# Kernel optimization log

Hardware: AMD Instinct MI355X
Metric: run time of the kernel (lower is better)

Reference implementation:

```python
import jax, jax.numpy as jnp
import numpy as np

B = 2
ROW, COL = 63, 84          # resolution
ROW_, COL_ = 32, 42        # resolution_
N = ROW * COL              # 5292 kv tokens
N_ = ROW_ * COL_           # 1344 q tokens
IN_DIM, OUT_DIM = 256, 512
KEY_DIM, NUM_HEADS, ATTN_RATIO, STRIDE = 16, 8, 2, 2
D = ATTN_RATIO * KEY_DIM   # 32 (value dim per head)
DH = D * NUM_HEADS         # 256
NH_KD = KEY_DIM * NUM_HEADS  # 128
H_KV = DH + NH_KD          # 384
SCALE = KEY_DIM ** -0.5
EPS = 1e-5


def _build_bias_idxs():
    # replicates the itertools.product double loop, vectorized; ids ordered by
    # first occurrence in row-major scan (same as dict insertion order).
    r_ = np.arange(ROW_); c_ = np.arange(COL_)
    r = np.arange(ROW); c = np.arange(COL)
    off_r = np.abs(r_[:, None] * STRIDE - r[None, :])      # (32, 63)
    off_c = np.abs(c_[:, None] * STRIDE - c[None, :])      # (42, 84)
    keys = (off_r[:, None, :, None] * 1000 + off_c[None, :, None, :]).reshape(-1)
    _, first_idx, inv = np.unique(keys, return_index=True, return_inverse=True)
    order = np.argsort(first_idx)
    rank = np.empty_like(order); rank[order] = np.arange(len(order))
    idxs = rank[inv].reshape(N_, N).astype(np.int32)
    return idxs, len(order)


def setup_inputs() -> dict:
    key = jax.random.key(0)
    ks = jax.random.split(key, 12)
    idxs_np, n_off = _build_bias_idxs()
    inp = {
        "x": jax.random.normal(ks[0], (B, N, IN_DIM), jnp.float32),
        "kv_w": jax.random.normal(ks[1], (H_KV, IN_DIM), jnp.float32) * (IN_DIM ** -0.5),
        "kv_g": jnp.ones((H_KV,), jnp.float32),
        "kv_b": jnp.zeros((H_KV,), jnp.float32),
        "q_w": jax.random.normal(ks[2], (NH_KD, IN_DIM), jnp.float32) * (IN_DIM ** -0.5),
        "q_g": jnp.ones((NH_KD,), jnp.float32),
        "q_b": jnp.zeros((NH_KD,), jnp.float32),
        "proj_w": jax.random.normal(ks[3], (OUT_DIM, DH), jnp.float32) * (DH ** -0.5),
        "proj_g": jnp.ones((OUT_DIM,), jnp.float32),
        "proj_b": jnp.zeros((OUT_DIM,), jnp.float32),
        "bias_table": jax.random.normal(ks[4], (NUM_HEADS, n_off), jnp.float32) * 0.02,
        "bias_idxs": jnp.asarray(idxs_np),
    }
    return inp


def _linear_bn(x, w, g, b):
    # Linear (no bias) followed by BatchNorm1d in training mode (batch stats
    # over flattened (B*N) dim, biased variance).
    y = jnp.einsum("bnc,oc->bno", x, w)
    flat = y.reshape(-1, y.shape[-1])
    mu = flat.mean(0)
    var = flat.var(0)
    return (y - mu) * (g / jnp.sqrt(var + EPS)) + b


def _hardswish(x):
    return x * jnp.clip(x + 3.0, 0.0, 6.0) / 6.0


def reference(x, kv_w, kv_g, kv_b, q_w, q_g, q_b, proj_w, proj_g, proj_b,
              bias_table, bias_idxs):
    Bx = x.shape[0]
    # kv projection -> split k (KEY_DIM) and v (D) per head
    kv = _linear_bn(x, kv_w, kv_g, kv_b).reshape(Bx, N, NUM_HEADS, KEY_DIM + D)
    k = kv[..., :KEY_DIM].transpose(0, 2, 1, 3)   # (B, H, N, key_dim)
    v = kv[..., KEY_DIM:].transpose(0, 2, 1, 3)   # (B, H, N, d)
    # q: spatial subsample then projection
    xs = x.reshape(Bx, ROW, COL, IN_DIM)[:, ::STRIDE, ::STRIDE].reshape(Bx, N_, IN_DIM)
    q = _linear_bn(xs, q_w, q_g, q_b).reshape(Bx, N_, NUM_HEADS, KEY_DIM).transpose(0, 2, 1, 3)
    # gathered relative position bias: (H, N_, N)
    ab = bias_table[:, bias_idxs]
    attn = jnp.einsum("bhqd,bhkd->bhqk", q, k) * SCALE + ab[None]
    attn = jax.nn.softmax(attn, axis=-1)
    out = jnp.einsum("bhqk,bhkd->bhqd", attn, v)       # (B, H, N_, d)
    out = out.transpose(0, 2, 1, 3).reshape(Bx, N_, DH)
    out = _linear_bn(_hardswish(out), proj_w, proj_g, proj_b)
    return out
```

## Files before the change

kernel.cpp:

```cpp
#include <hip/hip_runtime.h>
#include <hip/hip_bf16.h>
#include <math.h>

#define N_K 5292
#define N_KP 5376
#define N_Q 1344
#define NH_KD 128
#define NROWS 21504
#define LOG2E 1.4426950408889634f
#define MSTAT 16.0f

typedef float f32x4 __attribute__((ext_vector_type(4)));
typedef short short8 __attribute__((ext_vector_type(8)));

__device__ __forceinline__ float fexp2(float x) {
#if __has_builtin(__builtin_amdgcn_exp2f)
    return __builtin_amdgcn_exp2f(x);
#else
    return exp2f(x);
#endif
}

__device__ __forceinline__ unsigned pk_bf16(float a, float b) {
    union { __hip_bfloat162 h; unsigned u; } c;
    c.h = __float22bfloat162_rn(make_float2(a, b));
    return c.u;
}
__device__ __forceinline__ unsigned short f2bf(float a) {
    return (unsigned short)pk_bf16(a, 0.f);
}

__global__ __launch_bounds__(256) void prep_bf16(
    const float* __restrict__ X, const float* __restrict__ kv_w,
    const float* __restrict__ q_w,
    unsigned short* __restrict__ Xb, float* __restrict__ sums)
{
    int i = blockIdx.x * 256 + threadIdx.x;
    if (i >= 710144) {
        int j = i - 710144;
        float4 z = make_float4(0.f, 0.f, 0.f, 0.f);
        *(float4*)(sums + (size_t)j * 8)     = z;
        *(float4*)(sums + (size_t)j * 8 + 4) = z;
        return;
    }
    const float* src;
    long off;
    if (i < 677376)       { src = X;      off = i; }
    else if (i < 701952)  { src = kv_w;   off = i - 677376; }
    else                  { src = q_w;    off = i - 701952; }
    float4 v = *(const float4*)(src + off * 4);
    *(uint2*)(Xb + (size_t)i * 4) = make_uint2(pk_bf16(v.x, v.y), pk_bf16(v.z, v.w));
}

__device__ __forceinline__ void gemm_body_bb(
    const unsigned short* __restrict__ A, const unsigned short* __restrict__ W,
    long asrc, int nrow,
    unsigned short (*As)[40], unsigned short (*Bs)[40], f32x4 acc[4])
{
    const int t = threadIdx.x;
    const int w = t >> 6, lane = t & 63, g = lane >> 4, ln = lane & 15;
    const int srow = t >> 2;
    const int sc8 = (t & 3) * 8;

    uint4 a = make_uint4(0, 0, 0, 0);
    if (asrc >= 0) a = *(const uint4*)(A + asrc * 256 + sc8);
    uint4 b = *(const uint4*)(W + (size_t)nrow * 256 + sc8);

    #pragma unroll
    for (int k0 = 0; k0 < 256; k0 += 32) {
        __syncthreads();
        *(uint4*)&As[srow][sc8] = a;
        *(uint4*)&Bs[srow][sc8] = b;
        __syncthreads();

        if (k0 < 224) {
            if (asrc >= 0) a = *(const uint4*)(A + asrc * 256 + k0 + 32 + sc8);
            b = *(const uint4*)(W + (size_t)nrow * 256 + k0 + 32 + sc8);
        }

        short8 ah = *(const short8*)&As[w * 16 + ln][g * 8];
        #pragma unroll
        for (int nt = 0; nt < 4; ++nt) {
            short8 bh = *(const short8*)&Bs[nt * 16 + ln][g * 8];
            acc[nt] = __builtin_amdgcn_mfma_f32_16x16x32_bf16(ah, bh, acc[nt], 0, 0, 0);
        }
    }
}

__device__ __forceinline__ void gemm_stats(f32x4 acc[4], float* __restrict__ sums,
                                           int n0, int Ncols, float* scratch)
{
    const int t = threadIdx.x;
    const int w = t >> 6, lane = t & 63, g = lane >> 4, ln = lane & 15;
    float s4[4], q4[4];
    #pragma unroll
    for (int nt = 0; nt < 4; ++nt) {
        float s = acc[nt][0] + acc[nt][1] + acc[nt][2] + acc[nt][3];
        float q = fmaf(acc[nt][0], acc[nt][0], fmaf(acc[nt][1], acc[nt][1],
                  fmaf(acc[nt][2], acc[nt][2], acc[nt][3] * acc[nt][3])));
        s += __shfl_xor(s, 16); s += __shfl_xor(s, 32);
        q += __shfl_xor(q, 16); q += __shfl_xor(q, 32);
        s4[nt] = s; q4[nt] = q;
    }
    __syncthreads();
    float* st_s = scratch;
    float* st_q = scratch + 256;
    if (g == 0) {
        #pragma unroll
        for (int nt = 0; nt < 4; ++nt) {
            st_s[(w * 4 + nt) * 16 + ln] = s4[nt];
            st_q[(w * 4 + nt) * 16 + ln] = q4[nt];
        }
    }
    __syncthreads();
    if (t < 64) {
        int nt = t >> 4, c = t & 15;
        float a = 0.f, b2 = 0.f;
        #pragma unroll
        for (int ww = 0; ww < 4; ++ww) {
            a  += st_s[(ww * 4 + nt) * 16 + c];
            b2 += st_q[(ww * 4 + nt) * 16 + c];
        }
        atomicAdd(&sums[n0 + nt * 16 + c], a);
        atomicAdd(&sums[Ncols + n0 + nt * 16 + c], b2);
    }
}

__global__ __launch_bounds__(256) void gemm_qkv(
    const unsigned short* __restrict__ Xb, const unsigned short* __restrict__ kvWb,
    const unsigned short* __restrict__ qWb,
    const float* __restrict__ bias_table, const int* __restrict__ bias_idxs, int n_off,
    unsigned short* __restrict__ Kp, unsigned short* __restrict__ Vpt,
    float* __restrict__ bt_r,
    float* __restrict__ q_y, float* __restrict__ sums_kv, float* __restrict__ sums_q)
{
    __shared__ unsigned short As[64][40], Bs[64][40];
    const int t = threadIdx.x;
    const int w = t >> 6, lane = t & 63, g = lane >> 4, ln = lane & 15;
    const int srow = t >> 2;
    int id = blockIdx.x;

    if (id >= 1104) {
        id -= 1104;
        if (id < 168) {
            int i = id * 256 + t;
            int row = i / 84, j = i - row * 84;
            int slot;
            if (j < 20) {
                int kap = 44 + j;
                slot = 5248 + (((kap & 15) << 2) | (kap >> 4));
            } else {
                slot = 5312 + (j - 20);
            }
            Vpt[(size_t)row * N_KP + slot] = 0;
        } else {
            int i = (id - 168) * 256 + t;
            if (i < 8 * N_K) {
                int h = i / N_K, j = i - h * N_K;
                bt_r[i] = bias_table[h * n_off + bias_idxs[j]] * LOG2E;
            }
        }
        return;
    }

    f32x4 acc[4];
    #pragma unroll
    for (int nt = 0; nt < 4; ++nt) acc[nt] = (f32x4){0.f, 0.f, 0.f, 0.f};

    if (id < 1008) {
        const int xcd = id & 7, id8 = id >> 3;
        const int my = xcd + (id8 / 6) * 8, ny = id8 % 6;
        if (my >= 166) return;
        const int m0 = my * 64, n0 = ny * 64;
        int mrow = m0 + srow;
        long asrc = (mrow < 10584) ? mrow : -1;
        gemm_body_bb(Xb, kvWb, asrc, n0 + srow, As, Bs, acc);

        #pragma unroll
        for (int nt = 0; nt < 4; ++nt) {
            int c = n0 + nt * 16 + ln;
            int hh = c / 48, cc = c - 48 * hh;
            #pragma unroll
            for (int reg = 0; reg < 4; ++reg) {
                int mr = m0 + w * 16 + g * 4 + reg;
                if (mr < 10584) {
                    int bb = mr >= N_K;
                    int key = mr - bb * N_K;
                    unsigned short v16 = f2bf(acc[nt][reg]);
                    if (cc < 16) {
                        Kp[((size_t)(bb * 8 + hh) * N_K + key) * 16 + cc] = v16;
                    } else {
                        int kap = key & 63;
                        int keyp = (key & ~63) | (((kap & 15) << 2) | (kap >> 4));
                        Vpt[((size_t)(bb * 8 + hh) * 32 + cc - 16) * N_KP + keyp] = v16;
                    }
                }
            }
        }
        gemm_stats(acc, sums_kv, n0, 384, (float*)&As[0][0]);
    } else {
        id -= 1008;
        const int xcd = id & 7, id8 = id >> 3;
        const int my = xcd + (id8 / 2) * 8, ny = id8 % 2;
        if (my >= 42) return;
        const int m0 = my * 64, n0 = ny * 64;
        int mrow = m0 + srow;
        int bb = mrow / N_Q;
        int i = mrow - bb * N_Q;
        long asrc = (long)(bb * N_K + (i / 42) * 168 + (i % 42) * 2);
        gemm_body_bb(Xb, qWb, asrc, n0 + srow, As, Bs, acc);

        #pragma unroll
        for (int nt = 0; nt < 4; ++nt)
            #pragma unroll
            for (int reg = 0; reg < 4; ++reg) {
                int mr = m0 + w * 16 + g * 4 + reg;
                q_y[(size_t)mr * 128 + n0 + nt * 16 + ln] = acc[nt][reg];
            }
        gemm_stats(acc, sums_q, n0, 128, (float*)&As[0][0]);
    }
}

__global__ __launch_bounds__(256) void gemm_proj(
    const unsigned short* __restrict__ Ap, const unsigned short* __restrict__ Wp,
    float* __restrict__ Y, float* __restrict__ sums)
{
    __shared__ unsigned short As[64][40], Bs[64][40];
    const int t = threadIdx.x;
    const int w = t >> 6, lane = t & 63, g = lane >> 4, ln = lane & 15;
    const int id = blockIdx.x;
    const int xcd = id & 7, id8 = id >> 3;
    const int my = xcd + (id8 / 8) * 8, ny = id8 % 8;
    if (my >= 42) return;
    const int m0 = my * 64, n0 = ny * 64;

    f32x4 acc[4];
    #pragma unroll
    for (int nt = 0; nt < 4; ++nt) acc[nt] = (f32x4){0.f, 0.f, 0.f, 0.f};
    gemm_body_bb(Ap, Wp, m0 + (t >> 2), n0 + (t >> 2), As, Bs, acc);

    #pragma unroll
    for (int nt = 0; nt < 4; ++nt)
        #pragma unroll
        for (int reg = 0; reg < 4; ++reg) {
            int mr = m0 + w * 16 + g * 4 + reg;
            Y[(size_t)mr * 512 + n0 + nt * 16 + ln] = acc[nt][reg];
        }
    gemm_stats(acc, sums, n0, 512, (float*)&As[0][0]);
}

__global__ __launch_bounds__(256, 5) void attn_mfma(
    const unsigned short* __restrict__ Kp, const unsigned short* __restrict__ Vpt,
    const float* __restrict__ q_y, const float* __restrict__ sums_q,
    const float* __restrict__ q_g, const float* __restrict__ q_b,
    const float* __restrict__ sums_kv, const float* __restrict__ kv_g,
    const float* __restrict__ bt_r,
    float* __restrict__ pl, float* __restrict__ pacc)
{
    const int id = blockIdx.x;
    const int h = id & 7;
    const int z = (id >> 3) & 7;
    const int qt = id >> 6;
    const int b = z >> 2, ks = z & 3;
    const int t = threadIdx.x;
    const int w = t >> 6, lane = t & 63, g = lane >> 4, ln = lane & 15;

    __shared__ unsigned short btm_s[21 * 166];
    __shared__ unsigned short K_s[2][64][24];
    __shared__ unsigned short Vt_s[2][32][72];
    __shared__ unsigned short P_s[4][16][72];

    const int q0 = qt * 64;
    const int kstart = ks * 1344;
    const int kend = (kstart + 1344 < N_K) ? kstart + 1344 : N_K;
    const int ntiles = (kend - kstart + 63) >> 6;
    const bool tail = (ks == 3);

    const int kr0 = kstart / 84;
    const int kr1 = (kend - 1) / 84;
    const int rq2min = (q0 / 42) * 2;
    const int rq2max = ((q0 + 63) / 42) * 2;
    const int dmin_r = rq2min - kr1;
    const int rows = (rq2max - kr0) - dmin_r + 1;
    const int nb = rows * 166;
    const unsigned mxb = (unsigned)((nb - 1) * 2);
    {
        const float* src = bt_r + h * N_K;
        for (int j = t; j < nb; j += 256) {
            int rr = j / 166, ii = j - rr * 166;
            int dr = dmin_r + rr; dr = dr < 0 ? -dr : dr;
            int dc = ii - 83; dc = dc < 0 ? -dc : dc;
            btm_s[j] = f2bf(src[dr * 84 + dc]);
        }
    }

    short8 qfrag = (short8)0;
    if (lane < 32) {
        const float invq = 1.f / 2688.f, invk = 1.f / 10584.f;
        const float post = 0.25f * LOG2E;
        const int c0 = h * 16 + g * 8;
        const int ck = h * 48 + g * 8;
        const float* qp = q_y + (size_t)(b * N_Q + q0 + w * 16 + ln) * NH_KD + c0;
        float vv[8];
        #pragma unroll
        for (int j = 0; j < 8; ++j) {
            float mu  = sums_q[c0 + j] * invq;
            float var = fmaf(-mu, mu, sums_q[128 + c0 + j] * invq);
            float s   = q_g[c0 + j] * rsqrtf(var + 1e-5f) * post;
            float vq  = fmaf(qp[j], s, fmaf(-mu, s, q_b[c0 + j] * post));
            float muk = sums_kv[ck + j] * invk;
            float vrk = fmaf(-muk, muk, sums_kv[384 + ck + j] * invk);
            float sk  = kv_g[ck + j] * rsqrtf(vrk + 1e-5f);
            vv[j] = vq * sk;
        }
        union { short8 s; unsigned u[4]; } qf;
        qf.u[0] = pk_bf16(vv[0], vv[1]); qf.u[1] = pk_bf16(vv[2], vv[3]);
        qf.u[2] = pk_bf16(vv[4], vv[5]); qf.u[3] = pk_bf16(vv[6], vv[7]);
        qfrag = qf.s;
    }

    union { short8 s; unsigned u[4]; } onef;
    #pragma unroll
    for (int j = 0; j < 4; ++j) onef.u[j] = 0x3F803F80u;
    const short8 ones = onef.s;

    int baseb[4];
    #pragma unroll
    for (int reg = 0; reg < 4; ++reg) {
        int qg = q0 + w * 16 + g * 4 + reg;
        int rq2 = (qg / 42) * 2;
        int cq2 = (qg % 42) * 2;
        baseb[reg] = ((rq2 - dmin_r) * 166 + cq2 + 83) * 2;
    }
    int offb[4], kcc[4];
    #pragma unroll
    for (int st = 0; st < 4; ++st) {
        int kg = kstart + st * 16 + ln;
        int okr = kg / 84;
        kcc[st] = kg - okr * 84;
        offb[st] = -(okr * 166 + kcc[st]) * 2;
    }

    const unsigned* kp_base = (const unsigned*)Kp + (size_t)(b * 8 + h) * N_K * 8;
    const int skey = t >> 2, schunk = t & 3;
    const int vrow = t >> 3, vc8 = (t & 7) * 8;
    const unsigned short* vptr = Vpt + (size_t)(b * 8 + h) * 32 * N_KP
                                     + (size_t)vrow * N_KP + kstart + vc8;

    uint2 kreg; uint4 vreg;
    {
        int kg = kstart + skey; if (kg > N_K - 1) kg = N_K - 1;
        kreg = *(const uint2*)(kp_base + (size_t)kg * 8 + schunk * 2);
        vreg = *(const uint4*)vptr;
    }
    *(uint2*)&K_s[0][skey][schunk * 4] = kreg;
    *(uint4*)&Vt_s[0][vrow][vc8] = vreg;
    __syncthreads();

    f32x4 acc0 = {0.f, 0.f, 0.f, 0.f}, acc1 = {0.f, 0.f, 0.f, 0.f};
    f32x4 accL = {0.f, 0.f, 0.f, 0.f};
    const f32x4 minit = {-MSTAT, -MSTAT, -MSTAT, -MSTAT};
    int p = 0;

    for (int it = 0; it < ntiles; ++it) {
        const int k0 = kstart + it * 64;
        const bool notlast = (it + 1 < ntiles);
        if (notlast) {
            int kg = k0 + 64 + skey; if (kg > N_K - 1) kg = N_K - 1;
            kreg = *(const uint2*)(kp_base + (size_t)kg * 8 + schunk * 2);
            vreg = *(const uint4*)(vptr + 64);
        }

        f32x4 sf[4];
        #pragma unroll
        for (int st = 0; st < 4; ++st) {
            short8 bf = (short8)0;
            if (lane < 32) bf = *(const short8*)&K_s[p][st * 16 + ln][g * 8];
            sf[st] = __builtin_amdgcn_mfma_f32_16x16x32_bf16(qfrag, bf, minit, 0, 0, 0);
        }

        float pv[4][4];
        const bool clampit = tail && (it == ntiles - 1);
        if (!clampit) {
            #pragma unroll
            for (int st = 0; st < 4; ++st) {
                #pragma unroll
                for (int reg = 0; reg < 4; ++reg) {
                    unsigned ub = (unsigned)(baseb[reg] + offb[st]);
                    unsigned short bu = *(const unsigned short*)((const char*)btm_s + ub);
                    float bias = __uint_as_float(((unsigned)bu) << 16);
                    pv[st][reg] = fexp2(sf[st][reg] + bias);
                }
            }
        } else {
            #pragma unroll
            for (int st = 0; st < 4; ++st) {
                bool bad = (k0 + st * 16 + ln) >= N_K;
                #pragma unroll
                for (int reg = 0; reg < 4; ++reg) {
                    unsigned ub = (unsigned)(baseb[reg] + offb[st]);
                    ub = ub > mxb ? mxb : ub;
                    unsigned short bu = *(const unsigned short*)((const char*)btm_s + ub);
                    float bias = __uint_as_float(((unsigned)bu) << 16);
                    pv[st][reg] = bad ? 0.f : fexp2(sf[st][reg] + bias);
                }
            }
        }

        #pragma unroll
        for (int reg = 0; reg < 4; ++reg) {
            uint2 pw = make_uint2(pk_bf16(pv[0][reg], pv[1][reg]),
                                  pk_bf16(pv[2][reg], pv[3][reg]));
            *(uint2*)&P_s[w][g * 4 + reg][4 * ln] = pw;
        }
        __asm__ __volatile__("" ::: "memory");

        #pragma unroll
        for (int kt = 0; kt < 2; ++kt) {
            short8 af = *(const short8*)&P_s[w][ln][g * 8 + kt * 32];
            short8 b0 = *(const short8*)&Vt_s[p][ln][g * 8 + kt * 32];
            short8 b1 = *(const short8*)&Vt_s[p][ln + 16][g * 8 + kt * 32];
            acc0 = __builtin_amdgcn_mfma_f32_16x16x32_bf16(af, b0, acc0, 0, 0, 0);
            acc1 = __builtin_amdgcn_mfma_f32_16x16x32_bf16(af, b1, acc1, 0, 0, 0);
            accL = __builtin_amdgcn_mfma_f32_16x16x32_bf16(af, ones, accL, 0, 0, 0);
        }

        if (notlast) {
            int q2 = p ^ 1;
            *(uint2*)&K_s[q2][skey][schunk * 4] = kreg;
            *(uint4*)&Vt_s[q2][vrow][vc8] = vreg;
            __syncthreads();
            p = q2;
            vptr += 64;
        }

        #pragma unroll
        for (int st = 0; st < 4; ++st) {
            kcc[st] += 64;
            if (kcc[st] >= 84) { kcc[st] -= 84; offb[st] -= 292; }
            else offb[st] -= 128;
        }
    }

    const int rbase = (b * 8 + h) * N_Q + q0 + w * 16;
    #pragma unroll
    for (int reg = 0; reg < 4; ++reg) {
        int prow = ks * NROWS + rbase + g * 4 + reg;
        pacc[(size_t)prow * 32 + ln]      = acc0[reg];
        pacc[(size_t)prow * 32 + 16 + ln] = acc1[reg];
        if (ln == 0) pl[prow] = accL[reg];
    }
}

__global__ __launch_bounds__(256) void combine_kernel(const float* __restrict__ pl,
                                                      const float* __restrict__ pacc,
                                                      const float* __restrict__ sums_kv,
                                                      const float* __restrict__ kv_g,
                                                      const float* __restrict__ kv_b,
                                                      unsigned short* __restrict__ attn_o,
                                                      const float* __restrict__ proj_w,
                                                      unsigned short* __restrict__ projWb)
{
    if (blockIdx.x >= 672) {
        int i = (blockIdx.x - 672) * 256 + threadIdx.x;
        float4 v = *(const float4*)(proj_w + (size_t)i * 4);
        *(uint2*)(projWb + (size_t)i * 4) = make_uint2(pk_bf16(v.x, v.y), pk_bf16(v.z, v.w));
        return;
    }
    int idx = blockIdx.x * 256 + threadIdx.x;
    int r = idx >> 3, e4 = (idx & 7) * 4;
    float L = (pl[r] + pl[NROWS + r]) + (pl[2 * NROWS + r] + pl[3 * NROWS + r]);
    float invL = 1.f / L;
    size_t o = (size_t)r * 32 + e4;
    float4 v0 = *(const float4*)(pacc + o);
    float4 v1 = *(const float4*)(pacc + (size_t)NROWS * 32 + o);
    float4 v2 = *(const float4*)(pacc + (size_t)2 * NROWS * 32 + o);
    float4 v3 = *(const float4*)(pacc + (size_t)3 * NROWS * 32 + o);
    int q = r % N_Q;
    int bh = r / N_Q;
    int hh = bh & 7, b = bh >> 3;
    const int ch = hh * 48 + 16 + e4;
    const float invk = 1.f / 10584.f;
    float hs[4];
    #pragma unroll
    for (int u = 0; u < 4; ++u) {
        float v = (u == 0 ? v0.x + v1.x + v2.x + v3.x :
                   u == 1 ? v0.y + v1.y + v2.y + v3.y :
                   u == 2 ? v0.z + v1.z + v2.z + v3.z :
                            v0.w + v1.w + v2.w + v3.w);
        float mu  = sums_kv[ch + u] * invk;
        float var = fmaf(-mu, mu, sums_kv[384 + ch + u] * invk);
        float s   = kv_g[ch + u] * rsqrtf(var + 1e-5f);
        float tt  = fmaf(-mu, s, kv_b[ch + u]);
        v = fmaf(s, v * invL, tt);
        hs[u] = v * fminf(fmaxf(v + 3.f, 0.f), 6.f) * (1.f / 6.f);
    }
    *(uint2*)(attn_o + (size_t)(b * N_Q + q) * 256 + hh * 32 + e4) =
        make_uint2(pk_bf16(hs[0], hs[1]), pk_bf16(hs[2], hs[3]));
}

__global__ __launch_bounds__(256) void norm_apply(
    const float* __restrict__ Y, const float* __restrict__ sums,
    const float* __restrict__ g, const float* __restrict__ bb,
    float* __restrict__ out, int rows, int cols, float inv_rows)
{
    __shared__ float sc_s[64], sh_s[64];
    const int t = threadIdx.x;
    const int c0 = blockIdx.x * 64;
    if (t < 64) {
        int c = c0 + t;
        float mu  = sums[c] * inv_rows;
        float var = fmaf(-mu, mu, sums[cols + c] * inv_rows);
        float s   = g[c] * rsqrtf(var + 1e-5f);
        sc_s[t] = s;
        sh_s[t] = fmaf(-mu, s, bb[c]);
    }
    __syncthreads();
    const int c4 = (t & 15) * 4;
    float4 scv = *(const float4*)&sc_s[c4];
    float4 shv = *(const float4*)&sh_s[c4];
    for (int r = blockIdx.y * 16 + (t >> 4); r < rows; r += gridDim.y * 16) {
        size_t off = (size_t)r * cols + c0 + c4;
        float4 v = *(const float4*)(Y + off);
        v.x = fmaf(v.x, scv.x, shv.x);
        v.y = fmaf(v.y, scv.y, shv.y);
        v.z = fmaf(v.z, scv.z, shv.z);
        v.w = fmaf(v.w, scv.w, shv.w);
        *(float4*)(out + off) = v;
    }
}

extern "C" void kernel_launch(void* const* d_in, const int* in_sizes, int n_in,
                              void* d_out, int out_size, void* d_ws, size_t ws_size,
                              hipStream_t stream) {
    (void)n_in; (void)out_size; (void)ws_size;
    const float* x      = (const float*)d_in[0];
    const float* kv_w   = (const float*)d_in[1];
    const float* kv_g   = (const float*)d_in[2];
    const float* kv_b   = (const float*)d_in[3];
    const float* q_w    = (const float*)d_in[4];
    const float* q_g    = (const float*)d_in[5];
    const float* q_b    = (const float*)d_in[6];
    const float* proj_w = (const float*)d_in[7];
    const float* proj_g = (const float*)d_in[8];
    const float* proj_b = (const float*)d_in[9];
    const float* bias_table = (const float*)d_in[10];
    const int*   bias_idxs  = (const int*)d_in[11];
    const int    n_off = in_sizes[10] / 8;
    float* out = (float*)d_out;

    float* ws = (float*)d_ws;
    float* q_y  = ws;
    float* pacc = q_y + 2688 * 128;
    float* proj_y = pacc;
    float* pl = pacc + 4 * NROWS * 32;
    unsigned short* attn_o = (unsigned short*)(pl + 4 * NROWS);
    unsigned short* Kp  = attn_o + 2688 * 256;
    unsigned short* Vpt = Kp + 2 * 8 * N_K * 16;
    float* sums_kv = (float*)(Vpt + 2 * 8 * 32 * N_KP);
    float* sums_q  = sums_kv + 768;
    float* sums_p  = sums_q + 256;
    float* bt_r    = sums_p + 1024;

    unsigned short* Xb     = (unsigned short*)pacc;
    unsigned short* kvWb   = Xb + 10584 * 256;
    unsigned short* qWb    = kvWb + 384 * 256;
    unsigned short* projWb = (unsigned short*)q_y;

    prep_bf16<<<2775, 256, 0, stream>>>(x, kv_w, q_w, Xb, sums_kv);
    gemm_qkv<<<1104 + 168 + 166, 256, 0, stream>>>(Xb, kvWb, qWb, bias_table, bias_idxs,
                                                   n_off, Kp, Vpt, bt_r,
                                                   q_y, sums_kv, sums_q);
    attn_mfma<<<1344, 256, 0, stream>>>(Kp, Vpt, q_y, sums_q, q_g, q_b,
                                        sums_kv, kv_g, bt_r, pl, pacc);
    combine_kernel<<<672 + 128, 256, 0, stream>>>(pl, pacc, sums_kv, kv_g, kv_b, attn_o,
                                                  proj_w, projWb);
    gemm_proj<<<384, 256, 0, stream>>>(attn_o, projWb, proj_y, sums_p);
    norm_apply<<<dim3(8, 84), 256, 0, stream>>>(proj_y, sums_p, proj_g, proj_b, out,
                                                2688, 512, 1.f / 2688.f);
}
```

Measured before the change: 188.3 us.

## Use 128x128 GEMM tiles, fp32 bias table in LDS, lower attention occupancy hint

The QKV and projection GEMMs move from 64x64 tiles to 128x128 tiles with a 2x2 warp layout, so each wave issues 16 MFMAs per k-step and the grid shrinks. The column-stat reduction is adjusted to match. Separately, the attention kernel now keeps the relative-position bias in LDS as fp32 instead of bf16, which removes the conversion and improves precision but doubles LDS use. To compensate, its launch-bounds occupancy hint drops from 5 to 4. The larger tiles give the GEMMs fewer blocks (84 for proj), which risks underfilling the 256 CUs.

```diff
diff --git a/kernel.cpp b/kernel.cpp
--- a/kernel.cpp
+++ b/kernel.cpp
@@ -52,77 +52,96 @@
     *(uint2*)(Xb + (size_t)i * 4) = make_uint2(pk_bf16(v.x, v.y), pk_bf16(v.z, v.w));
 }
 
-__device__ __forceinline__ void gemm_body_bb(
+__device__ __forceinline__ void gemm_body128(
     const unsigned short* __restrict__ A, const unsigned short* __restrict__ W,
-    long asrc, int nrow,
-    unsigned short (*As)[40], unsigned short (*Bs)[40], f32x4 acc[4])
+    long asrc, long bsrc,
+    unsigned short (*As)[40], unsigned short (*Bs)[40], f32x4 acc[4][4])
 {
     const int t = threadIdx.x;
     const int w = t >> 6, lane = t & 63, g = lane >> 4, ln = lane & 15;
-    const int srow = t >> 2;
-    const int sc8 = (t & 3) * 8;
-
-    uint4 a = make_uint4(0, 0, 0, 0);
-    if (asrc >= 0) a = *(const uint4*)(A + asrc * 256 + sc8);
-    uint4 b = *(const uint4*)(W + (size_t)nrow * 256 + sc8);
+    const int wr = w >> 1, wc = w & 1;
+    const int srow = t >> 1;
+    const int sc16 = (t & 1) * 16;
+
+    uint4 a0 = make_uint4(0,0,0,0), a1 = make_uint4(0,0,0,0);
+    if (asrc >= 0) {
+        a0 = *(const uint4*)(A + asrc * 256 + sc16);
+        a1 = *(const uint4*)(A + asrc * 256 + sc16 + 8);
+    }
+    uint4 b0 = *(const uint4*)(W + bsrc * 256 + sc16);
+    uint4 b1 = *(const uint4*)(W + bsrc * 256 + sc16 + 8);
 
     #pragma unroll
     for (int k0 = 0; k0 < 256; k0 += 32) {
         __syncthreads();
-        *(uint4*)&As[srow][sc8] = a;
-        *(uint4*)&Bs[srow][sc8] = b;
+        *(uint4*)&As[srow][sc16]     = a0;
+        *(uint4*)&As[srow][sc16 + 8] = a1;
+        *(uint4*)&Bs[srow][sc16]     = b0;
+        *(uint4*)&Bs[srow][sc16 + 8] = b1;
         __syncthreads();
 
         if (k0 < 224) {
-            if (asrc >= 0) a = *(const uint4*)(A + asrc * 256 + k0 + 32 + sc8);
-            b = *(const uint4*)(W + (size_t)nrow * 256 + k0 + 32 + sc8);
-        }
-
-        short8 ah = *(const short8*)&As[w * 16 + ln][g * 8];
-        #pragma unroll
-        for (int nt = 0; nt < 4; ++nt) {
-            short8 bh = *(const short8*)&Bs[nt * 16 + ln][g * 8];
-            acc[nt] = __builtin_amdgcn_mfma_f32_16x16x32_bf16(ah, bh, acc[nt], 0, 0, 0);
-        }
-    }
-}
-
-__device__ __forceinline__ void gemm_stats(f32x4 acc[4], float* __restrict__ sums,
-                                           int n0, int Ncols, float* scratch)
+            if (asrc >= 0) {
+                a0 = *(const uint4*)(A + asrc * 256 + k0 + 32 + sc16);
+                a1 = *(const uint4*)(A + asrc * 256 + k0 + 32 + sc16 + 8);
+            }
+            b0 = *(const uint4*)(W + bsrc * 256 + k0 + 32 + sc16);
+            b1 = *(const uint4*)(W + bsrc * 256 + k0 + 32 + sc16 + 8);
+        }
+
+        short8 af[4], bf[4];
+        #pragma unroll
+        for (int mi = 0; mi < 4; ++mi)
+            af[mi] = *(const short8*)&As[wr * 64 + mi * 16 + ln][g * 8];
+        #pragma unroll
+        for (int ni = 0; ni < 4; ++ni)
+            bf[ni] = *(const short8*)&Bs[wc * 64 + ni * 16 + ln][g * 8];
+        #pragma unroll
+        for (int mi = 0; mi < 4; ++mi)
+            #pragma unroll
+            for (int ni = 0; ni < 4; ++ni)
+                acc[mi][ni] = __builtin_amdgcn_mfma_f32_16x16x32_bf16(
+                    af[mi], bf[ni], acc[mi][ni], 0, 0, 0);
+    }
+}
+
+__device__ __forceinline__ void gemm_stats128(f32x4 acc[4][4], float* __restrict__ sums,
+                                              int n0, int Ncols, float* scratch)
 {
     const int t = threadIdx.x;
     const int w = t >> 6, lane = t & 63, g = lane >> 4, ln = lane & 15;
-    float s4[4], q4[4];
-    #pragma unroll
-    for (int nt = 0; nt < 4; ++nt) {
-        float s = acc[nt][0] + acc[nt][1] + acc[nt][2] + acc[nt][3];
-        float q = fmaf(acc[nt][0], acc[nt][0], fmaf(acc[nt][1], acc[nt][1],
-                  fmaf(acc[nt][2], acc[nt][2], acc[nt][3] * acc[nt][3])));
+    float sA[4], qA[4];
+    #pragma unroll
+    for (int ni = 0; ni < 4; ++ni) {
+        float s = 0.f, q = 0.f;
+        #pragma unroll
+        for (int mi = 0; mi < 4; ++mi)
+            #pragma unroll
+            for (int r = 0; r < 4; ++r) {
+                float v = acc[mi][ni][r];
+                s += v; q = fmaf(v, v, q);
+            }
         s += __shfl_xor(s, 16); s += __shfl_xor(s, 32);
         q += __shfl_xor(q, 16); q += __shfl_xor(q, 32);
-        s4[nt] = s; q4[nt] = q;
+        sA[ni] = s; qA[ni] = q;
     }
     __syncthreads();
     float* st_s = scratch;
     float* st_q = scratch + 256;
     if (g == 0) {
         #pragma unroll
-        for (int nt = 0; nt < 4; ++nt) {
-            st_s[(w * 4 + nt) * 16 + ln] = s4[nt];
-            st_q[(w * 4 + nt) * 16 + ln] = q4[nt];
+        for (int ni = 0; ni < 4; ++ni) {
+            st_s[(w * 4 + ni) * 16 + ln] = sA[ni];
+            st_q[(w * 4 + ni) * 16 + ln] = qA[ni];
         }
     }
     __syncthreads();
-    if (t < 64) {
-        int nt = t >> 4, c = t & 15;
-        float a = 0.f, b2 = 0.f;
-        #pragma unroll
-        for (int ww = 0; ww < 4; ++ww) {
-            a  += st_s[(ww * 4 + nt) * 16 + c];
-            b2 += st_q[(ww * 4 + nt) * 16 + c];
-        }
-        atomicAdd(&sums[n0 + nt * 16 + c], a);
-        atomicAdd(&sums[Ncols + n0 + nt * 16 + c], b2);
+    if (t < 128) {
+        int wc = t >> 6, nl = t & 63;
+        float a  = st_s[wc * 64 + nl] + st_s[(wc + 2) * 64 + nl];
+        float b2 = st_q[wc * 64 + nl] + st_q[(wc + 2) * 64 + nl];
+        atomicAdd(&sums[n0 + t], a);
+        atomicAdd(&sums[Ncols + n0 + t], b2);
     }
 }
 
@@ -134,14 +153,15 @@
     float* __restrict__ bt_r,
     float* __restrict__ q_y, float* __restrict__ sums_kv, float* __restrict__ sums_q)
 {
-    __shared__ unsigned short As[64][40], Bs[64][40];
+    __shared__ unsigned short As[128][40], Bs[128][40];
     const int t = threadIdx.x;
     const int w = t >> 6, lane = t & 63, g = lane >> 4, ln = lane & 15;
-    const int srow = t >> 2;
+    const int wr = w >> 1, wc = w & 1;
+    const int srow = t >> 1;
     int id = blockIdx.x;
 
-    if (id >= 1104) {
-        id -= 1104;
+    if (id >= 270) {
+        id -= 270;
         if (id < 168) {
             int i = id * 256 + t;
             int row = i / 84, j = i - row * 84;
@@ -163,61 +183,65 @@
         return;
     }
 
-    f32x4 acc[4];
-    #pragma unroll
-    for (int nt = 0; nt < 4; ++nt) acc[nt] = (f32x4){0.f, 0.f, 0.f, 0.f};
-
-    if (id < 1008) {
-        const int xcd = id & 7, id8 = id >> 3;
-        const int my = xcd + (id8 / 6) * 8, ny = id8 % 6;
-        if (my >= 166) return;
-        const int m0 = my * 64, n0 = ny * 64;
+    f32x4 acc[4][4];
+    #pragma unroll
+    for (int mi = 0; mi < 4; ++mi)
+        #pragma unroll
+        for (int ni = 0; ni < 4; ++ni) acc[mi][ni] = (f32x4){0.f, 0.f, 0.f, 0.f};
+
+    if (id < 249) {
+        const int my = id / 3, ny = id % 3;
+        const int m0 = my * 128, n0 = ny * 128;
         int mrow = m0 + srow;
         long asrc = (mrow < 10584) ? mrow : -1;
-        gemm_body_bb(Xb, kvWb, asrc, n0 + srow, As, Bs, acc);
-
-        #pragma unroll
-        for (int nt = 0; nt < 4; ++nt) {
-            int c = n0 + nt * 16 + ln;
+        gemm_body128(Xb, kvWb, asrc, n0 + srow, As, Bs, acc);
+
+        #pragma unroll
+        for (int ni = 0; ni < 4; ++ni) {
+            int c = n0 + wc * 64 + ni * 16 + ln;
             int hh = c / 48, cc = c - 48 * hh;
             #pragma unroll
-            for (int reg = 0; reg < 4; ++reg) {
-                int mr = m0 + w * 16 + g * 4 + reg;
-                if (mr < 10584) {
-                    int bb = mr >= N_K;
-                    int key = mr - bb * N_K;
-                    unsigned short v16 = f2bf(acc[nt][reg]);
-                    if (cc < 16) {
-                        Kp[((size_t)(bb * 8 + hh) * N_K + key) * 16 + cc] = v16;
-                    } else {
-                        int kap = key & 63;
-                        int keyp = (key & ~63) | (((kap & 15) << 2) | (kap >> 4));
-                        Vpt[((size_t)(bb * 8 + hh) * 32 + cc - 16) * N_KP + keyp] = v16;
+            for (int mi = 0; mi < 4; ++mi) {
+                #pragma unroll
+                for (int reg = 0; reg < 4; ++reg) {
+                    int mr = m0 + wr * 64 + mi * 16 + g * 4 + reg;
+                    if (mr < 10584) {
+                        int bb = mr >= N_K;
+                        int key = mr - bb * N_K;
+                        unsigned short v16 = f2bf(acc[mi][ni][reg]);
+                        if (cc < 16) {
+                            Kp[((size_t)(bb * 8 + hh) * N_K + key) * 16 + cc] = v16;
+                        } else {
+                            int kap = key & 63;
+                            int keyp = (key & ~63) | (((kap & 15) << 2) | (kap >> 4));
+                            Vpt[((size_t)(bb * 8 + hh) * 32 + cc - 16) * N_KP + keyp] = v16;
+                        }
                     }
                 }
             }
         }
-        gemm_stats(acc, sums_kv, n0, 384, (float*)&As[0][0]);
+        gemm_stats128(acc, sums_kv, n0, 384, (float*)&As[0][0]);
     } else {
-        id -= 1008;
-        const int xcd = id & 7, id8 = id >> 3;
-        const int my = xcd + (id8 / 2) * 8, ny = id8 % 2;
-        if (my >= 42) return;
-        const int m0 = my * 64, n0 = ny * 64;
+        const int my = id - 249;
+        const int m0 = my * 128;
         int mrow = m0 + srow;
         int bb = mrow / N_Q;
         int i = mrow - bb * N_Q;
         long asrc = (long)(bb * N_K + (i / 42) * 168 + (i % 42) * 2);
-        gemm_body_bb(Xb, qWb, asrc, n0 + srow, As, Bs, acc);
-
-        #pragma unroll
-        for (int nt = 0; nt < 4; ++nt)
+        gemm_body128(Xb, qWb, asrc, srow, As, Bs, acc);
+
+        #pragma unroll
+        for (int ni = 0; ni < 4; ++ni) {
+            int c = wc * 64 + ni * 16 + ln;
             #pragma unroll
-            for (int reg = 0; reg < 4; ++reg) {
-                int mr = m0 + w * 16 + g * 4 + reg;
-                q_y[(size_t)mr * 128 + n0 + nt * 16 + ln] = acc[nt][reg];
-            }
-        gemm_stats(acc, sums_q, n0, 128, (float*)&As[0][0]);
+            for (int mi = 0; mi < 4; ++mi)
+                #pragma unroll
+                for (int reg = 0; reg < 4; ++reg) {
+                    int mr = m0 + wr * 64 + mi * 16 + g * 4 + reg;
+                    q_y[(size_t)mr * 128 + c] = acc[mi][ni][reg];
+                }
+        }
+        gemm_stats128(acc, sums_q, 0, 128, (float*)&As[0][0]);
     }
 }
 
@@ -225,31 +249,36 @@
     const unsigned short* __restrict__ Ap, const unsigned short* __restrict__ Wp,
     float* __restrict__ Y, float* __restrict__ sums)
 {
-    __shared__ unsigned short As[64][40], Bs[64][40];
+    __shared__ unsigned short As[128][40], Bs[128][40];
     const int t = threadIdx.x;
     const int w = t >> 6, lane = t & 63, g = lane >> 4, ln = lane & 15;
-    const int id = blockIdx.x;
-    const int xcd = id & 7, id8 = id >> 3;
-    const int my = xcd + (id8 / 8) * 8, ny = id8 % 8;
-    if (my >= 42) return;
-    const int m0 = my * 64, n0 = ny * 64;
-
-    f32x4 acc[4];
-    #pragma unroll
-    for (int nt = 0; nt < 4; ++nt) acc[nt] = (f32x4){0.f, 0.f, 0.f, 0.f};
-    gemm_body_bb(Ap, Wp, m0 + (t >> 2), n0 + (t >> 2), As, Bs, acc);
-
-    #pragma unroll
-    for (int nt = 0; nt < 4; ++nt)
-        #pragma unroll
-        for (int reg = 0; reg < 4; ++reg) {
-            int mr = m0 + w * 16 + g * 4 + reg;
-            Y[(size_t)mr * 512 + n0 + nt * 16 + ln] = acc[nt][reg];
-        }
-    gemm_stats(acc, sums, n0, 512, (float*)&As[0][0]);
-}
-
-__global__ __launch_bounds__(256, 5) void attn_mfma(
+    const int wr = w >> 1, wc = w & 1;
+    const int srow = t >> 1;
+    const int my = blockIdx.x / 4, ny = blockIdx.x % 4;
+    const int m0 = my * 128, n0 = ny * 128;
+
+    f32x4 acc[4][4];
+    #pragma unroll
+    for (int mi = 0; mi < 4; ++mi)
+        #pragma unroll
+        for (int ni = 0; ni < 4; ++ni) acc[mi][ni] = (f32x4){0.f, 0.f, 0.f, 0.f};
+    gemm_body128(Ap, Wp, m0 + srow, n0 + srow, As, Bs, acc);
+
+    #pragma unroll
+    for (int ni = 0; ni < 4; ++ni) {
+        int c = n0 + wc * 64 + ni * 16 + ln;
+        #pragma unroll
+        for (int mi = 0; mi < 4; ++mi)
+            #pragma unroll
+            for (int reg = 0; reg < 4; ++reg) {
+                int mr = m0 + wr * 64 + mi * 16 + g * 4 + reg;
+                Y[(size_t)mr * 512 + c] = acc[mi][ni][reg];
+            }
+    }
+    gemm_stats128(acc, sums, n0, 512, (float*)&As[0][0]);
+}
+
+__global__ __launch_bounds__(256, 4) void attn_mfma(
     const unsigned short* __restrict__ Kp, const unsigned short* __restrict__ Vpt,
     const float* __restrict__ q_y, const float* __restrict__ sums_q,
     const float* __restrict__ q_g, const float* __restrict__ q_b,
@@ -265,7 +294,7 @@
     const int t = threadIdx.x;
     const int w = t >> 6, lane = t & 63, g = lane >> 4, ln = lane & 15;
 
-    __shared__ unsigned short btm_s[21 * 166];
+    __shared__ float btm_s[21 * 166];
     __shared__ unsigned short K_s[2][64][24];
     __shared__ unsigned short Vt_s[2][32][72];
     __shared__ unsigned short P_s[4][16][72];
@@ -283,14 +312,14 @@
     const int dmin_r = rq2min - kr1;
     const int rows = (rq2max - kr0) - dmin_r + 1;
     const int nb = rows * 166;
-    const unsigned mxb = (unsigned)((nb - 1) * 2);
+    const unsigned mxb = (unsigned)((nb - 1) * 4);
     {
         const float* src = bt_r + h * N_K;
         for (int j = t; j < nb; j += 256) {
             int rr = j / 166, ii = j - rr * 166;
             int dr = dmin_r + rr; dr = dr < 0 ? -dr : dr;
             int dc = ii - 83; dc = dc < 0 ? -dc : dc;
-            btm_s[j] = f2bf(src[dr * 84 + dc]);
+            btm_s[j] = src[dr * 84 + dc];
         }
     }
 
@@ -330,7 +359,7 @@
         int qg = q0 + w * 16 + g * 4 + reg;
         int rq2 = (qg / 42) * 2;
         int cq2 = (qg % 42) * 2;
-        baseb[reg] = ((rq2 - dmin_r) * 166 + cq2 + 83) * 2;
+        baseb[reg] = ((rq2 - dmin_r) * 166 + cq2 + 83) * 4;
     }
     int offb[4], kcc[4];
     #pragma unroll
@@ -338,7 +367,7 @@
         int kg = kstart + st * 16 + ln;
         int okr = kg / 84;
         kcc[st] = kg - okr * 84;
-        offb[st] = -(okr * 166 + kcc[st]) * 2;
+        offb[st] = -(okr * 166 + kcc[st]) * 4;
     }
 
     const unsigned* kp_base = (const unsigned*)Kp + (size_t)(b * 8 + h) * N_K * 8;
@@ -387,8 +416,7 @@
                 #pragma unroll
                 for (int reg = 0; reg < 4; ++reg) {
                     unsigned ub = (unsigned)(baseb[reg] + offb[st]);
-                    unsigned short bu = *(const unsigned short*)((const char*)btm_s + ub);
-                    float bias = __uint_as_float(((unsigned)bu) << 16);
+                    float bias = *(const float*)((const char*)btm_s + ub);
                     pv[st][reg] = fexp2(sf[st][reg] + bias);
                 }
             }
@@ -400,8 +428,7 @@
                 for (int reg = 0; reg < 4; ++reg) {
                     unsigned ub = (unsigned)(baseb[reg] + offb[st]);
                     ub = ub > mxb ? mxb : ub;
-                    unsigned short bu = *(const unsigned short*)((const char*)btm_s + ub);
-                    float bias = __uint_as_float(((unsigned)bu) << 16);
+                    float bias = *(const float*)((const char*)btm_s + ub);
                     pv[st][reg] = bad ? 0.f : fexp2(sf[st][reg] + bias);
                 }
             }
@@ -437,8 +464,8 @@
         #pragma unroll
         for (int st = 0; st < 4; ++st) {
             kcc[st] += 64;
-            if (kcc[st] >= 84) { kcc[st] -= 84; offb[st] -= 292; }
-            else offb[st] -= 128;
+            if (kcc[st] >= 84) { kcc[st] -= 84; offb[st] -= 584; }
+            else offb[st] -= 256;
         }
     }
 
@@ -568,14 +595,14 @@
     unsigned short* projWb = (unsigned short*)q_y;
 
     prep_bf16<<<2775, 256, 0, stream>>>(x, kv_w, q_w, Xb, sums_kv);
-    gemm_qkv<<<1104 + 168 + 166, 256, 0, stream>>>(Xb, kvWb, qWb, bias_table, bias_idxs,
-                                                   n_off, Kp, Vpt, bt_r,
-                                                   q_y, sums_kv, sums_q);
+    gemm_qkv<<<270 + 168 + 166, 256, 0, stream>>>(Xb, kvWb, qWb, bias_table, bias_idxs,
+                                                  n_off, Kp, Vpt, bt_r,
+                                                  q_y, sums_kv, sums_q);
     attn_mfma<<<1344, 256, 0, stream>>>(Kp, Vpt, q_y, sums_q, q_g, q_b,
                                         sums_kv, kv_g, bt_r, pl, pacc);
     combine_kernel<<<672 + 128, 256, 0, stream>>>(pl, pacc, sums_kv, kv_g, kv_b, attn_o,
                                                   proj_w, projWb);
-    gemm_proj<<<384, 256, 0, stream>>>(attn_o, projWb, proj_y, sums_p);
+    gemm_proj<<<84, 256, 0, stream>>>(attn_o, projWb, proj_y, sums_p);
     norm_apply<<<dim3(8, 84), 256, 0, stream>>>(proj_y, sums_p, proj_g, proj_b, out,
                                                 2688, 512, 1.f / 2688.f);
 }
```

Measured after the change: 189.4 us. Within noise of the previous version (+0.6%).
